# Kernel optimization log

Hardware: AMD Instinct MI355X
Metric: run time of the kernel (lower is better)

Reference implementation:

```python
import jax, jax.numpy as jnp
import numpy as np

B, M, N, K = 256, 512, 512, 128
ALPHA = 0.0025  # a_scale * b_scale (per-tensor dequant factor)


def setup_inputs() -> dict:
    key = jax.random.key(0)
    k1, k2 = jax.random.split(key)
    # int8 quantized activations; 'a' row-major [B, M, K], 'b' stored as [B, N, K]
    a = jax.random.randint(k1, (B, M, K), -128, 128, dtype=jnp.int8)
    b = jax.random.randint(k2, (B, N, K), -128, 128, dtype=jnp.int8)
    alpha = jnp.float32(ALPHA)
    return {"a": a, "b": b, "alpha": alpha}


def reference(a, b, alpha):
    # with fused per-tensor scale dequant to fp32 in the epilogue.
    # out[b, m, n] = alpha * sum_k a[b, m, k] * b[b, n, k]
    acc = jnp.einsum(
        "bmk,bnk->bmn",
        a.astype(jnp.int32),
        b.astype(jnp.int32),
    )  # [B, M, N] int32 accumulator
    return acc.astype(jnp.float32) * alpha
```

## Files before the change

### kernel.cpp

```cpp
#include <hip/hip_runtime.h>
#include <stdint.h>

#define BATCH 256
#define M 512
#define N 512
#define K 128

typedef int int4v __attribute__((ext_vector_type(4)));

__global__ __launch_bounds__(512, 2) void bmm_s8s8_f32_kernel(
    const int* __restrict__ A32,
    const int* __restrict__ B32,
    const float* __restrict__ alpha_p,
    float* __restrict__ O)
{
    __shared__ int8_t As[M * K];
    __shared__ int8_t Bs[N * K];

    const int tid = threadIdx.x;
    const int bat = blockIdx.x;

    const int* Ag = A32 + (size_t)bat * (M * K);
    const int* Bg = B32 + (size_t)bat * (N * K);

#pragma unroll 4
    for (int i = 0; i < 32; ++i) {
        const int g   = i * 512 + tid;
        const int row = g >> 5;
        const int kg  = g & 31;
        const int kc  = kg >> 2;
        const int sub = kg & 3;
        const int kcs = kc ^ (row & 7);

        int4v wa = *(const int4v*)(Ag + (size_t)g * 4);
        int4v wb = *(const int4v*)(Bg + (size_t)g * 4);
        const int pa = (wa.x & 0xff) | ((wa.y & 0xff) << 8) |
                       ((wa.z & 0xff) << 16) | (wa.w << 24);
        const int pb = (wb.x & 0xff) | ((wb.y & 0xff) << 8) |
                       ((wb.z & 0xff) << 16) | (wb.w << 24);
        *(int*)(As + row * 128 + kcs * 16 + sub * 4) = pa;
        *(int*)(Bs + row * 128 + kcs * 16 + sub * 4) = pb;
    }
    __syncthreads();

    const int lane = tid & 63;
    const int wave = tid >> 6;
    const int l15  = lane & 15;
    const int quad = lane >> 4;
    const int sn   = wave;

    int4v bf[2][4];
#pragma unroll
    for (int ks = 0; ks < 2; ++ks)
#pragma unroll
        for (int j = 0; j < 4; ++j) {
            const int rb = sn * 64 + j * 16 + l15;
            const int kc = (ks * 4 + quad) ^ (rb & 7);
            bf[ks][j] = *(const int4v*)(Bs + rb * 128 + kc * 16);
        }

    const float alpha = *alpha_p;

    for (int sm = 0; sm < 8; ++sm) {
        int4v af[2][4];
#pragma unroll
        for (int ks = 0; ks < 2; ++ks)
#pragma unroll
            for (int i = 0; i < 4; ++i) {
                const int ra = sm * 64 + i * 16 + l15;
                const int kc = (ks * 4 + quad) ^ (ra & 7);
                af[ks][i] = *(const int4v*)(As + ra * 128 + kc * 16);
            }

        int4v acc[4][4];
#pragma unroll
        for (int i = 0; i < 4; ++i)
#pragma unroll
            for (int j = 0; j < 4; ++j)
                acc[i][j] = (int4v){0, 0, 0, 0};

#pragma unroll
        for (int ks = 0; ks < 2; ++ks)
#pragma unroll
            for (int i = 0; i < 4; ++i)
#pragma unroll
                for (int j = 0; j < 4; ++j)
                    acc[i][j] = __builtin_amdgcn_mfma_i32_16x16x64_i8(
                        af[ks][i], bf[ks][j], acc[i][j], 0, 0, 0);

        float* Ob = O + ((size_t)bat * M + sm * 64 + quad * 4) * N + sn * 64 + l15;
#pragma unroll
        for (int i = 0; i < 4; ++i)
#pragma unroll
            for (int r = 0; r < 4; ++r) {
                float* rowp = Ob + (size_t)(i * 16 + r) * N;
#pragma unroll
                for (int j = 0; j < 4; ++j)
                    rowp[j * 16] = alpha * (float)acc[i][j][r];
            }
    }
}

extern "C" void kernel_launch(void* const* d_in, const int* in_sizes, int n_in,
                              void* d_out, int out_size, void* d_ws, size_t ws_size,
                              hipStream_t stream) {
    const int*   a     = (const int*)d_in[0];
    const int*   b     = (const int*)d_in[1];
    const float* alpha = (const float*)d_in[2];
    float*       out   = (float*)d_out;

    dim3 grid(BATCH);
    dim3 block(512);
    bmm_s8s8_f32_kernel<<<grid, block, 0, stream>>>(a, b, alpha, out);
}
```

Baseline: 361.3 us.

## Tile batched int8 GEMM into 128x128 blocks with transposed MFMA for vector stores

Replaces the one-block-per-batch kernel (512 threads staging the full 512x128 A and B into 128 KB of LDS) with a 3D grid of 128x128 output tiles per batch. Each block uses 256 threads and 32 KB of LDS. The MFMA operands are swapped so each lane holds four consecutive N columns, which allows float4 output stores in place of scalar strided stores. This raises block count and occupancy. In exchange, each A and B row is loaded and repacked from global memory four times instead of once.

Result: slower. 381.7 us (+5.7%).

```diff
diff --git a/kernel.cpp b/kernel.cpp
--- a/kernel.cpp
+++ b/kernel.cpp
@@ -7,30 +7,31 @@
 #define K 128
 
 typedef int int4v __attribute__((ext_vector_type(4)));
+typedef float float4v __attribute__((ext_vector_type(4)));
 
-__global__ __launch_bounds__(512, 2) void bmm_s8s8_f32_kernel(
+__global__ __launch_bounds__(256, 3) void bmm_s8s8_f32_kernel(
     const int* __restrict__ A32,
     const int* __restrict__ B32,
     const float* __restrict__ alpha_p,
     float* __restrict__ O)
 {
-    __shared__ int8_t As[M * K];
-    __shared__ int8_t Bs[N * K];
+    __shared__ int8_t As[128 * 128];
+    __shared__ int8_t Bs[128 * 128];
 
     const int tid = threadIdx.x;
-    const int bat = blockIdx.x;
+    const int bat = blockIdx.z;
+    const int mt0 = blockIdx.y * 128;
+    const int nt0 = blockIdx.x * 128;
 
-    const int* Ag = A32 + (size_t)bat * (M * K);
-    const int* Bg = B32 + (size_t)bat * (N * K);
+    const int* Ag = A32 + ((size_t)bat * M + mt0) * K;
+    const int* Bg = B32 + ((size_t)bat * N + nt0) * K;
 
 #pragma unroll 4
-    for (int i = 0; i < 32; ++i) {
-        const int g   = i * 512 + tid;
+    for (int i = 0; i < 16; ++i) {
+        const int g   = i * 256 + tid;
         const int row = g >> 5;
-        const int kg  = g & 31;
-        const int kc  = kg >> 2;
-        const int sub = kg & 3;
-        const int kcs = kc ^ (row & 7);
+        const int d   = g & 31;
+        const int loff = row * 128 + (((d >> 2) ^ (row & 7)) << 4) + (d & 3) * 4;
 
         int4v wa = *(const int4v*)(Ag + (size_t)g * 4);
         int4v wb = *(const int4v*)(Bg + (size_t)g * 4);
@@ -38,66 +39,61 @@
                        ((wa.z & 0xff) << 16) | (wa.w << 24);
         const int pb = (wb.x & 0xff) | ((wb.y & 0xff) << 8) |
                        ((wb.z & 0xff) << 16) | (wb.w << 24);
-        *(int*)(As + row * 128 + kcs * 16 + sub * 4) = pa;
-        *(int*)(Bs + row * 128 + kcs * 16 + sub * 4) = pb;
+        *(int*)(As + loff) = pa;
+        *(int*)(Bs + loff) = pb;
     }
     __syncthreads();
 
     const int lane = tid & 63;
     const int wave = tid >> 6;
+    const int wm   = (wave >> 1) * 64;
+    const int wn   = (wave & 1) * 64;
     const int l15  = lane & 15;
     const int quad = lane >> 4;
-    const int sn   = wave;
 
-    int4v bf[2][4];
+    int4v af[2][4], bf[2][4];
 #pragma unroll
     for (int ks = 0; ks < 2; ++ks)
 #pragma unroll
-        for (int j = 0; j < 4; ++j) {
-            const int rb = sn * 64 + j * 16 + l15;
-            const int kc = (ks * 4 + quad) ^ (rb & 7);
-            bf[ks][j] = *(const int4v*)(Bs + rb * 128 + kc * 16);
+        for (int i = 0; i < 4; ++i) {
+            const int ra = wm + i * 16 + l15;
+            const int rb = wn + i * 16 + l15;
+            const int kca = (ks * 4 + quad) ^ (ra & 7);
+            const int kcb = (ks * 4 + quad) ^ (rb & 7);
+            af[ks][i] = *(const int4v*)(As + ra * 128 + kca * 16);
+            bf[ks][i] = *(const int4v*)(Bs + rb * 128 + kcb * 16);
         }
 
-    const float alpha = *alpha_p;
+    int4v acc[4][4];
+#pragma unroll
+    for (int i = 0; i < 4; ++i)
+#pragma unroll
+        for (int j = 0; j < 4; ++j)
+            acc[i][j] = (int4v){0, 0, 0, 0};
 
-    for (int sm = 0; sm < 8; ++sm) {
-        int4v af[2][4];
 #pragma unroll
-        for (int ks = 0; ks < 2; ++ks)
-#pragma unroll
-            for (int i = 0; i < 4; ++i) {
-                const int ra = sm * 64 + i * 16 + l15;
-                const int kc = (ks * 4 + quad) ^ (ra & 7);
-                af[ks][i] = *(const int4v*)(As + ra * 128 + kc * 16);
-            }
-
-        int4v acc[4][4];
+    for (int ks = 0; ks < 2; ++ks)
 #pragma unroll
         for (int i = 0; i < 4; ++i)
 #pragma unroll
             for (int j = 0; j < 4; ++j)
-                acc[i][j] = (int4v){0, 0, 0, 0};
+                acc[i][j] = __builtin_amdgcn_mfma_i32_16x16x64_i8(
+                    bf[ks][j], af[ks][i], acc[i][j], 0, 0, 0);
 
+    const float alpha = *alpha_p;
+    float* Ob = O + ((size_t)bat * M + mt0 + wm + l15) * N + nt0 + wn + quad * 4;
 #pragma unroll
-        for (int ks = 0; ks < 2; ++ks)
+    for (int i = 0; i < 4; ++i) {
+        float* rowp = Ob + (size_t)(i * 16) * N;
 #pragma unroll
-            for (int i = 0; i < 4; ++i)
-#pragma unroll
-                for (int j = 0; j < 4; ++j)
-                    acc[i][j] = __builtin_amdgcn_mfma_i32_16x16x64_i8(
-                        af[ks][i], bf[ks][j], acc[i][j], 0, 0, 0);
-
-        float* Ob = O + ((size_t)bat * M + sm * 64 + quad * 4) * N + sn * 64 + l15;
-#pragma unroll
-        for (int i = 0; i < 4; ++i)
-#pragma unroll
-            for (int r = 0; r < 4; ++r) {
-                float* rowp = Ob + (size_t)(i * 16 + r) * N;
-#pragma unroll
-                for (int j = 0; j < 4; ++j)
-                    rowp[j * 16] = alpha * (float)acc[i][j][r];
-            }
+        for (int j = 0; j < 4; ++j) {
+            float4v v;
+            v.x = alpha * (float)acc[i][j][0];
+            v.y = alpha * (float)acc[i][j][1];
+            v.z = alpha * (float)acc[i][j][2];
+            v.w = alpha * (float)acc[i][j][3];
+            *(float4v*)(rowp + j * 16) = v;
+        }
     }
 }
 
@@ -109,7 +105,7 @@
     const float* alpha = (const float*)d_in[2];
     float*       out   = (float*)d_out;
 
-    dim3 grid(BATCH);
-    dim3 block(512);
+    dim3 grid(N / 128, M / 128, BATCH);
+    dim3 block(256);
     bmm_s8s8_f32_kernel<<<grid, block, 0, stream>>>(a, b, alpha, out);
 }
```
